# Kernel tuning notes

Measured on AMD Instinct MI355X. Metric: run time of the kernel, lower is better.

## Reference

```python
import jax, jax.numpy as jnp
import numpy as np

N = 100000   # nodes
E = 3200000  # edges
D = 256      # node_dim
H = 64       # hidden (conv1 out)
L = 64       # latent_dim
G = 128      # graphs in batch


def _gcn_conv(x, src, dst, W, b):
    """PyG GCNConv with edge_weight=1: add self-loops, sym deg-norm, scatter-add."""
    n = x.shape[0]
    loop = jnp.arange(n)
    s = jnp.concatenate([src, loop])
    d = jnp.concatenate([dst, loop])
    w = jnp.ones(s.shape[0], x.dtype)
    deg = jax.ops.segment_sum(w, d, num_segments=n)
    dinv = jnp.where(deg > 0, jax.lax.rsqrt(deg), 0.0)
    norm = dinv[s] * w * dinv[d]                      # [E+N]
    h = x @ W                                         # lin (no bias)
    out = jax.ops.segment_sum(h[s] * norm[:, None], d, num_segments=n)
    return out + b


def _mean_pool(z, batch, num_graphs):
    zsum = jax.ops.segment_sum(z, batch, num_segments=num_graphs)
    cnt = jax.ops.segment_sum(jnp.ones(z.shape[0], z.dtype), batch, num_segments=num_graphs)
    return zsum / jnp.clip(cnt, 1.0)[:, None]


def setup_inputs() -> dict:
    key = jax.random.key(0)
    ks = jax.random.split(key, 8)
    x = jax.random.normal(ks[0], (N, D), jnp.float32)
    edge_index = jax.random.randint(ks[1], (2, E), 0, N, dtype=jnp.int64)
    batch = jnp.sort(jax.random.randint(ks[2], (N,), 0, G, dtype=jnp.int64))
    glorot = lambda k, fi, fo: jax.random.normal(k, (fi, fo), jnp.float32) / np.sqrt(fi).astype(np.float32)
    return {
        "x": x, "edge_index": edge_index, "batch": batch,
        "W1": glorot(ks[3], D, H), "b1": jnp.zeros((H,), jnp.float32),
        "W2": glorot(ks[4], H, L), "b2": jnp.zeros((L,), jnp.float32),
        "Wd1": glorot(ks[5], L, 64), "bd1": jnp.zeros((64,), jnp.float32),
        "Wd2": glorot(ks[6], 64, D), "bd2": jnp.zeros((D,), jnp.float32),
    }


def reference(x, edge_index, batch, W1, b1, W2, b2, Wd1, bd1, Wd2, bd2):
    src, dst = edge_index[0], edge_index[1]
    h = jax.nn.relu(_gcn_conv(x, src, dst, W1, b1))
    z = _gcn_conv(h, src, dst, W2, b2)
    z_pool = _mean_pool(z, batch, G)                  # [G, L]
    x_hat = jax.nn.relu(z_pool @ Wd1 + bd1) @ Wd2 + bd2  # [G, D]
    return (x_hat, z_pool)
```

## Files before the change

### kernel.cpp

```cpp
#include <hip/hip_runtime.h>
#include <hip/hip_bf16.h>
#include <hip/hip_fp16.h>
#include <hip/hip_fp8.h>

namespace {
constexpr int kN = 100000;
constexpr int kE = 3200000;
constexpr int kD = 256;
constexpr int kH = 64;
constexpr int kG = 128;

constexpr int kNB   = 782;
constexpr int kCapS = 4608;
constexpr int kCap  = 64;
constexpr int kNPad = 100352;

constexpr size_t kSlBytes = (size_t)(kN + 1) * 32;

constexpr size_t kAlign = 512;
constexpr size_t align_up(size_t v) { return (v + kAlign - 1) & ~(kAlign - 1); }

constexpr size_t OFF_CURD = 0;
constexpr size_t OFF_GCNT = OFF_CURD + align_up(kNB * 4);
constexpr size_t OFF_QRAW = OFF_GCNT + kAlign;
constexpr size_t ZERO_BYTES = OFF_QRAW + align_up((size_t)kG * kH * 4);
constexpr size_t OFF_CNT  = ZERO_BYTES;
constexpr size_t OFF_DINV = OFF_CNT + align_up((size_t)kNPad * 4);
constexpr size_t OFF_SD   = OFF_DINV + align_up((size_t)kNPad * 4);
constexpr size_t OFF_REC  = OFF_SD + align_up((size_t)kNB * kCapS * 4);
constexpr size_t OFF_HL   = OFF_REC + align_up((size_t)kNPad * kCap * 4);
constexpr size_t OFF_H2   = OFF_HL + align_up(2 * kSlBytes);
}

__device__ __forceinline__ unsigned pack4_fp8(float a, float b, float c, float d) {
#if __has_builtin(__builtin_amdgcn_cvt_pk_fp8_f32)
    int r = 0;
    r = __builtin_amdgcn_cvt_pk_fp8_f32(a, b, r, false);
    r = __builtin_amdgcn_cvt_pk_fp8_f32(c, d, r, true);
    return (unsigned)r;
#else
    __hip_fp8_e4m3 qa(a), qb(b), qc(c), qd(d);
    return (unsigned)qa.__x | ((unsigned)qb.__x << 8)
         | ((unsigned)qc.__x << 16) | ((unsigned)qd.__x << 24);
#endif
}

__device__ __forceinline__ void add4q(float (&acc)[4], unsigned u) {
#if __has_builtin(__builtin_amdgcn_cvt_pk_f32_fp8)
    typedef float v2f __attribute__((ext_vector_type(2)));
    v2f f0 = __builtin_amdgcn_cvt_pk_f32_fp8((int)u, false);
    v2f f1 = __builtin_amdgcn_cvt_pk_f32_fp8((int)u, true);
    acc[0] += f0.x; acc[1] += f0.y; acc[2] += f1.x; acc[3] += f1.y;
#else
    #pragma unroll
    for (int j = 0; j < 4; ++j) {
        __hip_fp8_e4m3 v; v.__x = (__hip_fp8_storage_t)((u >> (8 * j)) & 0xFF);
        acc[j] += (float)v;
    }
#endif
}

__global__ __launch_bounds__(1024) void k_bucket(const int* __restrict__ src,
                                                 const int* __restrict__ dst,
                                                 int* __restrict__ curD,
                                                 unsigned* __restrict__ streamD) {
    __shared__ int cD[kNB], bD[kNB];
    int t = threadIdx.x;
    for (int i = t; i < kNB; i += 1024) cD[i] = 0;
    __syncthreads();
    int e0 = blockIdx.x * 16384;
    #pragma unroll
    for (int k = 0; k < 16; ++k) {
        int e = e0 + k * 1024 + t;
        if (e < kE) atomicAdd(&cD[dst[e] >> 7], 1);
    }
    __syncthreads();
    for (int i = t; i < kNB; i += 1024)
        bD[i] = cD[i] ? atomicAdd(&curD[i], cD[i]) : 0;
    __syncthreads();
    for (int i = t; i < kNB; i += 1024) cD[i] = 0;
    __syncthreads();
    #pragma unroll
    for (int k = 0; k < 16; ++k) {
        int e = e0 + k * 1024 + t;
        if (e < kE) {
            int s = src[e], d = dst[e];
            int pd = bD[d >> 7] + atomicAdd(&cD[d >> 7], 1);
            if (pd < kCapS)
                streamD[(size_t)(d >> 7) * kCapS + pd] =
                    ((unsigned)(d & 127) << 17) | (unsigned)s;
        }
    }
}

__global__ __launch_bounds__(256) void k_fillB(const int* __restrict__ curD,
                                               const unsigned* __restrict__ streamD,
                                               int* __restrict__ rec,
                                               int* __restrict__ cnt) {
    __shared__ int lc[128];
    int b = blockIdx.x, t = threadIdx.x;
    if (t < 128) lc[t] = 0;
    __syncthreads();
    int n = min(curD[b], kCapS);
    const unsigned* sp = streamD + (size_t)b * kCapS;
    for (int i = t; i < n; i += 256) {
        unsigned u = sp[i];
        int dlo = (u >> 17) & 127;
        int slot = atomicAdd(&lc[dlo], 1);
        if (slot < kCap)
            rec[((((size_t)b << 7) | dlo) << 6) + slot] = (int)(u & 0x1FFFF);
    }
    __syncthreads();
    if (t < 128) {
        int d = (b << 7) + t;
        if (d < kNPad) cnt[d] = lc[t];
    }
}

__global__ void k_gcnt(const int* __restrict__ batch, int* __restrict__ gcnt) {
    __shared__ int h[kG];
    int t = threadIdx.x;
    if (t < kG) h[t] = 0;
    __syncthreads();
    for (int i = blockIdx.x * blockDim.x + t; i < kN; i += gridDim.x * blockDim.x)
        atomicAdd(&h[batch[i]], 1);
    __syncthreads();
    if (t < kG && h[t]) atomicAdd(&gcnt[t], h[t]);
}

__global__ void k_dinv(const int* __restrict__ cnt, float* __restrict__ dinv,
                       unsigned* __restrict__ hl8, unsigned* __restrict__ h8) {
    int i = blockIdx.x * blockDim.x + threadIdx.x;
    if (i < kN) dinv[i] = rsqrtf((float)(cnt[i] + 1));
    if (blockIdx.x == 0 && threadIdx.x < 32) {
        int t = threadIdx.x;
        unsigned* p = (t < 16) ? hl8 : h8;
        int s = (t >> 3) & 1;
        int j = t & 7;
        p[(s * kSlBytes) / 4 + (size_t)kN * 8 + j] = 0u;
    }
}

__global__ __launch_bounds__(256) void k_gemm1(const float* __restrict__ x,
                                               const float* __restrict__ W1,
                                               const float* __restrict__ dinv,
                                               unsigned char* __restrict__ hl8) {
    constexpr int TM = 64;
    constexpr int KC = 32;
    __shared__ float xs[TM][36];
    __shared__ float ws[KC][kH];
    int t = threadIdx.x;
    int tx = t & 15;
    int ty = t >> 4;
    int nb = blockIdx.x * TM;
    float acc[4][4] = {};
    for (int k0 = 0; k0 < kD; k0 += KC) {
        #pragma unroll
        for (int j = 0; j < 2; ++j) {
            int id = t * 2 + j;
            int row = id >> 3;
            int c4 = (id & 7) * 4;
            int node = nb + row;
            if (node >= kN) node = kN - 1;
            float4 v = *(const float4*)(x + (size_t)node * kD + k0 + c4);
            *(float4*)&xs[row][c4] = v;
        }
        #pragma unroll
        for (int j = 0; j < 2; ++j) {
            int id = t * 2 + j;
            int row = id >> 4;
            int c4 = (id & 15) * 4;
            float4 v = *(const float4*)(W1 + (size_t)(k0 + row) * kH + c4);
            *(float4*)&ws[row][c4] = v;
        }
        __syncthreads();
        #pragma unroll
        for (int kk = 0; kk < KC; ++kk) {
            float a0 = xs[ty * 4 + 0][kk];
            float a1 = xs[ty * 4 + 1][kk];
            float a2 = xs[ty * 4 + 2][kk];
            float a3 = xs[ty * 4 + 3][kk];
            float4 b = *(const float4*)&ws[kk][tx * 4];
            acc[0][0] = fmaf(a0, b.x, acc[0][0]); acc[0][1] = fmaf(a0, b.y, acc[0][1]);
            acc[0][2] = fmaf(a0, b.z, acc[0][2]); acc[0][3] = fmaf(a0, b.w, acc[0][3]);
            acc[1][0] = fmaf(a1, b.x, acc[1][0]); acc[1][1] = fmaf(a1, b.y, acc[1][1]);
            acc[1][2] = fmaf(a1, b.z, acc[1][2]); acc[1][3] = fmaf(a1, b.w, acc[1][3]);
            acc[2][0] = fmaf(a2, b.x, acc[2][0]); acc[2][1] = fmaf(a2, b.y, acc[2][1]);
            acc[2][2] = fmaf(a2, b.z, acc[2][2]); acc[2][3] = fmaf(a2, b.w, acc[2][3]);
            acc[3][0] = fmaf(a3, b.x, acc[3][0]); acc[3][1] = fmaf(a3, b.y, acc[3][1]);
            acc[3][2] = fmaf(a3, b.z, acc[3][2]); acc[3][3] = fmaf(a3, b.w, acc[3][3]);
        }
        __syncthreads();
    }
    int slice = tx >> 3;
    int off = (tx & 7) * 4;
    #pragma unroll
    for (int i = 0; i < 4; ++i) {
        int node = nb + ty * 4 + i;
        if (node < kN) {
            float di = dinv[node];
            unsigned p = pack4_fp8(di * acc[i][0], di * acc[i][1],
                                   di * acc[i][2], di * acc[i][3]);
            *(unsigned*)(hl8 + slice * kSlBytes + (size_t)node * 32 + off) = p;
        }
    }
}

__global__ __launch_bounds__(256) void k_conv1(const int* __restrict__ rec,
                                               const int* __restrict__ cnt,
                                               const float* __restrict__ dinv,
                                               const unsigned char* __restrict__ hl8,
                                               const float* __restrict__ b1,
                                               unsigned char* __restrict__ h8) {
    int tid = threadIdx.x;
    int lane = tid & 63;
    int slice = blockIdx.x & 1;
    int node = (blockIdx.x >> 1) * 4 + (tid >> 6);
    if (node >= kN) return;
    int slot = lane >> 3;
    int fl = lane & 7;
    const unsigned char* hsl = hl8 + slice * kSlBytes;
    size_t base = (size_t)node << 6;
    int len = min(cnt[node], kCap);
    float a0[4] = {}, a1[4] = {};
    for (int c0 = 0; c0 < len; c0 += 16) {
        int e0 = c0 + slot;
        int e1 = c0 + 8 + slot;
        int s0 = (e0 < len) ? rec[base + e0] : kN;
        int s1 = (e1 < len) ? rec[base + e1] : kN;
        unsigned v0 = *(const unsigned*)(hsl + (size_t)s0 * 32 + fl * 4);
        unsigned v1 = *(const unsigned*)(hsl + (size_t)s1 * 32 + fl * 4);
        add4q(a0, v0);
        add4q(a1, v1);
    }
    #pragma unroll
    for (int j = 0; j < 4; ++j) a0[j] += a1[j];
    #pragma unroll
    for (int d = 8; d < 64; d <<= 1) {
        #pragma unroll
        for (int j = 0; j < 4; ++j) a0[j] += __shfl_xor(a0[j], d, 64);
    }
    if (slot == 0) {
        unsigned sv = *(const unsigned*)(hsl + (size_t)node * 32 + fl * 4);
        add4q(a0, sv);
        float di = dinv[node];
        float4 bz = *(const float4*)(b1 + slice * 32 + fl * 4);
        float r0 = di * fmaxf(fmaf(di, a0[0], bz.x), 0.f);
        float r1 = di * fmaxf(fmaf(di, a0[1], bz.y), 0.f);
        float r2 = di * fmaxf(fmaf(di, a0[2], bz.z), 0.f);
        float r3 = di * fmaxf(fmaf(di, a0[3], bz.w), 0.f);
        unsigned o = pack4_fp8(r0, r1, r2, r3);
        *(unsigned*)(h8 + slice * kSlBytes + (size_t)node * 32 + fl * 4) = o;
    }
}

__global__ __launch_bounds__(256) void k_pool3(const int* __restrict__ rec,
                                               const int* __restrict__ cnt,
                                               const float* __restrict__ dinv,
                                               const unsigned char* __restrict__ h8,
                                               const int* __restrict__ batch,
                                               float* __restrict__ q_raw) {
    constexpr int CHUNK = 8;
    int tid = threadIdx.x;
    int lane = tid & 63;
    int slice = blockIdx.x & 1;
    int wid = (blockIdx.x >> 1) * 4 + (tid >> 6);
    int n0 = wid * CHUNK;
    if (n0 >= kN) return;
    int n1 = n0 + CHUNK; if (n1 > kN) n1 = kN;
    int slot = lane >> 3;
    int fl = lane & 7;
    const unsigned char* hsl = h8 + slice * kSlBytes;
    float racc[4] = {};
    int gcur = batch[n0];
    for (int i = n0; i < n1; ++i) {
        int g = batch[i];
        if (g != gcur) {
            #pragma unroll
            for (int d = 8; d < 64; d <<= 1) {
                #pragma unroll
                for (int j = 0; j < 4; ++j) racc[j] += __shfl_xor(racc[j], d, 64);
            }
            if (lane < 8) {
                #pragma unroll
                for (int j = 0; j < 4; ++j)
                    atomicAdd(&q_raw[(gcur << 6) + slice * 32 + fl * 4 + j], racc[j]);
            }
            #pragma unroll
            for (int j = 0; j < 4; ++j) racc[j] = 0.f;
            gcur = g;
        }
        size_t base = (size_t)i << 6;
        int len = min(cnt[i], kCap);
        float ns0[4] = {}, ns1[4] = {};
        for (int c0 = 0; c0 < len; c0 += 16) {
            int e0 = c0 + slot;
            int e1 = c0 + 8 + slot;
            int s0 = (e0 < len) ? rec[base + e0] : kN;
            int s1 = (e1 < len) ? rec[base + e1] : kN;
            unsigned v0 = *(const unsigned*)(hsl + (size_t)s0 * 32 + fl * 4);
            unsigned v1 = *(const unsigned*)(hsl + (size_t)s1 * 32 + fl * 4);
            add4q(ns0, v0);
            add4q(ns1, v1);
        }
        if (slot == 0) {
            unsigned sv = *(const unsigned*)(hsl + (size_t)i * 32 + fl * 4);
            add4q(ns0, sv);
        }
        float di = dinv[i];
        #pragma unroll
        for (int j = 0; j < 4; ++j) racc[j] = fmaf(di, ns0[j] + ns1[j], racc[j]);
    }
    #pragma unroll
    for (int d = 8; d < 64; d <<= 1) {
        #pragma unroll
        for (int j = 0; j < 4; ++j) racc[j] += __shfl_xor(racc[j], d, 64);
    }
    if (lane < 8) {
        #pragma unroll
        for (int j = 0; j < 4; ++j)
            atomicAdd(&q_raw[(gcur << 6) + slice * 32 + fl * 4 + j], racc[j]);
    }
}

__global__ __launch_bounds__(64) void k_head(const float* __restrict__ q_raw,
                                             const int* __restrict__ gcnt,
                                             const float* __restrict__ W2,
                                             const float* __restrict__ b2,
                                             const float* __restrict__ Wd1,
                                             const float* __restrict__ bd1,
                                             const float* __restrict__ Wd2,
                                             const float* __restrict__ bd2,
                                             float* __restrict__ out) {
    __shared__ float zm[kH], zp[kH], tt[kH];
    int g = blockIdx.x, c = threadIdx.x;
    int cg = gcnt[g];
    float inv = (cg > 0) ? 1.f / (float)cg : 0.f;
    zm[c] = q_raw[(size_t)g * kH + c] * inv;
    __syncthreads();
    float a = b2[c];
    #pragma unroll 8
    for (int k = 0; k < kH; ++k) a = fmaf(zm[k], W2[k * kH + c], a);
    if (cg == 0) a = 0.f;
    out[(size_t)kG * kD + (size_t)g * kH + c] = a;
    zp[c] = a;
    __syncthreads();
    float t = bd1[c];
    #pragma unroll 8
    for (int k = 0; k < kH; ++k) t = fmaf(zp[k], Wd1[k * 64 + c], t);
    tt[c] = fmaxf(t, 0.f);
    __syncthreads();
    #pragma unroll
    for (int j4 = 0; j4 < 4; ++j4) {
        int col = c + j4 * 64;
        float v = bd2[col];
        #pragma unroll 8
        for (int k = 0; k < 64; ++k) v = fmaf(tt[k], Wd2[k * kD + col], v);
        out[(size_t)g * kD + col] = v;
    }
}

extern "C" void kernel_launch(void* const* d_in, const int* in_sizes, int n_in,
                              void* d_out, int out_size, void* d_ws, size_t ws_size,
                              hipStream_t stream) {
    const float* x    = (const float*)d_in[0];
    const int*   ei   = (const int*)d_in[1];
    const int*   src  = ei;
    const int*   dst  = ei + kE;
    const int*   batch= (const int*)d_in[2];
    const float* W1   = (const float*)d_in[3];
    const float* b1   = (const float*)d_in[4];
    const float* W2   = (const float*)d_in[5];
    const float* b2   = (const float*)d_in[6];
    const float* Wd1  = (const float*)d_in[7];
    const float* bd1  = (const float*)d_in[8];
    const float* Wd2  = (const float*)d_in[9];
    const float* bd2  = (const float*)d_in[10];
    float* out = (float*)d_out;

    char* ws = (char*)d_ws;
    int*           curD  = (int*)(ws + OFF_CURD);
    int*           gcnt  = (int*)(ws + OFF_GCNT);
    float*         q_raw = (float*)(ws + OFF_QRAW);
    int*           cnt   = (int*)(ws + OFF_CNT);
    float*         dinv  = (float*)(ws + OFF_DINV);
    unsigned*      sD    = (unsigned*)(ws + OFF_SD);
    int*           rec   = (int*)(ws + OFF_REC);
    unsigned char* hl8   = (unsigned char*)(ws + OFF_HL);
    unsigned char* h8    = (unsigned char*)(ws + OFF_H2);

    hipMemsetAsync(d_ws, 0, ZERO_BYTES, stream);

    const int nBucketBlocks = (kE + 16383) / 16384;

    k_bucket<<<nBucketBlocks, 1024, 0, stream>>>(src, dst, curD, sD);
    k_fillB<<<kNB, 256, 0, stream>>>(curD, sD, rec, cnt);

    k_gcnt<<<128, 256, 0, stream>>>(batch, gcnt);
    k_dinv<<<(kN + 255) / 256, 256, 0, stream>>>(cnt, dinv,
                                                 (unsigned*)hl8, (unsigned*)h8);

    k_gemm1<<<(kN + 63) / 64, 256, 0, stream>>>(x, W1, dinv, hl8);

    k_conv1<<<((kN + 3) / 4) * 2, 256, 0, stream>>>(rec, cnt, dinv, hl8, b1, h8);

    const int nPoolWaves = (kN + 7) / 8;
    k_pool3<<<((nPoolWaves + 3) / 4) * 2, 256, 0, stream>>>(rec, cnt, dinv, h8, batch, q_raw);

    k_head<<<kG, 64, 0, stream>>>(q_raw, gcnt, W2, b2, Wd1, bd1, Wd2, bd2, out);
}
```

Measured before the change: 319.1 us.

## Store conv1 input as unsliced 64-byte fp8 rows and gather full rows

```diff
diff --git a/kernel.cpp b/kernel.cpp
--- a/kernel.cpp
+++ b/kernel.cpp
@@ -29,7 +29,7 @@
 constexpr size_t OFF_SD   = OFF_DINV + align_up((size_t)kNPad * 4);
 constexpr size_t OFF_REC  = OFF_SD + align_up((size_t)kNB * kCapS * 4);
 constexpr size_t OFF_HL   = OFF_REC + align_up((size_t)kNPad * kCap * 4);
-constexpr size_t OFF_H2   = OFF_HL + align_up(2 * kSlBytes);
+constexpr size_t OFF_H2   = OFF_HL + align_up((size_t)(kN + 1) * kH);
 }
 
 __device__ __forceinline__ unsigned pack4_fp8(float a, float b, float c, float d) {
@@ -60,6 +60,13 @@
 #endif
 }
 
+__device__ __forceinline__ void add8q(float (&acc)[8], uint2 u) {
+    float* a0 = acc;
+    float* a1 = acc + 4;
+    add4q(*(float(*)[4])a0, u.x);
+    add4q(*(float(*)[4])a1, u.y);
+}
+
 __global__ __launch_bounds__(1024) void k_bucket(const int* __restrict__ src,
                                                  const int* __restrict__ dst,
                                                  int* __restrict__ curD,
@@ -134,10 +141,13 @@
     if (i < kN) dinv[i] = rsqrtf((float)(cnt[i] + 1));
     if (blockIdx.x == 0 && threadIdx.x < 32) {
         int t = threadIdx.x;
-        unsigned* p = (t < 16) ? hl8 : h8;
-        int s = (t >> 3) & 1;
-        int j = t & 7;
-        p[(s * kSlBytes) / 4 + (size_t)kN * 8 + j] = 0u;
+        if (t < 16) {
+            hl8[(size_t)kN * 16 + t] = 0u;
+        } else {
+            int s = (t >> 3) & 1;
+            int j = t & 7;
+            h8[(s * kSlBytes) / 4 + (size_t)kN * 8 + j] = 0u;
+        }
     }
 }
 
@@ -147,7 +157,7 @@
                                                unsigned char* __restrict__ hl8) {
     constexpr int TM = 64;
     constexpr int KC = 32;
-    __shared__ float xs[TM][36];
+    __shared__ float xs[KC][TM + 4];
     __shared__ float ws[KC][kH];
     int t = threadIdx.x;
     int tx = t & 15;
@@ -163,7 +173,10 @@
             int node = nb + row;
             if (node >= kN) node = kN - 1;
             float4 v = *(const float4*)(x + (size_t)node * kD + k0 + c4);
-            *(float4*)&xs[row][c4] = v;
+            xs[c4 + 0][row] = v.x;
+            xs[c4 + 1][row] = v.y;
+            xs[c4 + 2][row] = v.z;
+            xs[c4 + 3][row] = v.w;
         }
         #pragma unroll
         for (int j = 0; j < 2; ++j) {
@@ -176,24 +189,19 @@
         __syncthreads();
         #pragma unroll
         for (int kk = 0; kk < KC; ++kk) {
-            float a0 = xs[ty * 4 + 0][kk];
-            float a1 = xs[ty * 4 + 1][kk];
-            float a2 = xs[ty * 4 + 2][kk];
-            float a3 = xs[ty * 4 + 3][kk];
+            float4 a = *(const float4*)&xs[kk][ty * 4];
             float4 b = *(const float4*)&ws[kk][tx * 4];
-            acc[0][0] = fmaf(a0, b.x, acc[0][0]); acc[0][1] = fmaf(a0, b.y, acc[0][1]);
-            acc[0][2] = fmaf(a0, b.z, acc[0][2]); acc[0][3] = fmaf(a0, b.w, acc[0][3]);
-            acc[1][0] = fmaf(a1, b.x, acc[1][0]); acc[1][1] = fmaf(a1, b.y, acc[1][1]);
-            acc[1][2] = fmaf(a1, b.z, acc[1][2]); acc[1][3] = fmaf(a1, b.w, acc[1][3]);
-            acc[2][0] = fmaf(a2, b.x, acc[2][0]); acc[2][1] = fmaf(a2, b.y, acc[2][1]);
-            acc[2][2] = fmaf(a2, b.z, acc[2][2]); acc[2][3] = fmaf(a2, b.w, acc[2][3]);
-            acc[3][0] = fmaf(a3, b.x, acc[3][0]); acc[3][1] = fmaf(a3, b.y, acc[3][1]);
-            acc[3][2] = fmaf(a3, b.z, acc[3][2]); acc[3][3] = fmaf(a3, b.w, acc[3][3]);
+            acc[0][0] = fmaf(a.x, b.x, acc[0][0]); acc[0][1] = fmaf(a.x, b.y, acc[0][1]);
+            acc[0][2] = fmaf(a.x, b.z, acc[0][2]); acc[0][3] = fmaf(a.x, b.w, acc[0][3]);
+            acc[1][0] = fmaf(a.y, b.x, acc[1][0]); acc[1][1] = fmaf(a.y, b.y, acc[1][1]);
+            acc[1][2] = fmaf(a.y, b.z, acc[1][2]); acc[1][3] = fmaf(a.y, b.w, acc[1][3]);
+            acc[2][0] = fmaf(a.z, b.x, acc[2][0]); acc[2][1] = fmaf(a.z, b.y, acc[2][1]);
+            acc[2][2] = fmaf(a.z, b.z, acc[2][2]); acc[2][3] = fmaf(a.z, b.w, acc[2][3]);
+            acc[3][0] = fmaf(a.w, b.x, acc[3][0]); acc[3][1] = fmaf(a.w, b.y, acc[3][1]);
+            acc[3][2] = fmaf(a.w, b.z, acc[3][2]); acc[3][3] = fmaf(a.w, b.w, acc[3][3]);
         }
         __syncthreads();
     }
-    int slice = tx >> 3;
-    int off = (tx & 7) * 4;
     #pragma unroll
     for (int i = 0; i < 4; ++i) {
         int node = nb + ty * 4 + i;
@@ -201,7 +209,7 @@
             float di = dinv[node];
             unsigned p = pack4_fp8(di * acc[i][0], di * acc[i][1],
                                    di * acc[i][2], di * acc[i][3]);
-            *(unsigned*)(hl8 + slice * kSlBytes + (size_t)node * 32 + off) = p;
+            *(unsigned*)(hl8 + (size_t)node * kH + tx * 4) = p;
         }
     }
 }
@@ -214,43 +222,45 @@
                                                unsigned char* __restrict__ h8) {
     int tid = threadIdx.x;
     int lane = tid & 63;
-    int slice = blockIdx.x & 1;
-    int node = (blockIdx.x >> 1) * 4 + (tid >> 6);
+    int node = blockIdx.x * 4 + (tid >> 6);
     if (node >= kN) return;
     int slot = lane >> 3;
     int fl = lane & 7;
-    const unsigned char* hsl = hl8 + slice * kSlBytes;
     size_t base = (size_t)node << 6;
     int len = min(cnt[node], kCap);
-    float a0[4] = {}, a1[4] = {};
+    float acc0[8] = {}, acc1[8] = {};
     for (int c0 = 0; c0 < len; c0 += 16) {
         int e0 = c0 + slot;
         int e1 = c0 + 8 + slot;
         int s0 = (e0 < len) ? rec[base + e0] : kN;
         int s1 = (e1 < len) ? rec[base + e1] : kN;
-        unsigned v0 = *(const unsigned*)(hsl + (size_t)s0 * 32 + fl * 4);
-        unsigned v1 = *(const unsigned*)(hsl + (size_t)s1 * 32 + fl * 4);
-        add4q(a0, v0);
-        add4q(a1, v1);
-    }
-    #pragma unroll
-    for (int j = 0; j < 4; ++j) a0[j] += a1[j];
+        uint2 v0 = *(const uint2*)(hl8 + ((size_t)s0 << 6) + fl * 8);
+        uint2 v1 = *(const uint2*)(hl8 + ((size_t)s1 << 6) + fl * 8);
+        add8q(acc0, v0);
+        add8q(acc1, v1);
+    }
+    #pragma unroll
+    for (int j = 0; j < 8; ++j) acc0[j] += acc1[j];
     #pragma unroll
     for (int d = 8; d < 64; d <<= 1) {
         #pragma unroll
-        for (int j = 0; j < 4; ++j) a0[j] += __shfl_xor(a0[j], d, 64);
+        for (int j = 0; j < 8; ++j) acc0[j] += __shfl_xor(acc0[j], d, 64);
     }
     if (slot == 0) {
-        unsigned sv = *(const unsigned*)(hsl + (size_t)node * 32 + fl * 4);
-        add4q(a0, sv);
+        uint2 sv = *(const uint2*)(hl8 + ((size_t)node << 6) + fl * 8);
+        add8q(acc0, sv);
         float di = dinv[node];
-        float4 bz = *(const float4*)(b1 + slice * 32 + fl * 4);
-        float r0 = di * fmaxf(fmaf(di, a0[0], bz.x), 0.f);
-        float r1 = di * fmaxf(fmaf(di, a0[1], bz.y), 0.f);
-        float r2 = di * fmaxf(fmaf(di, a0[2], bz.z), 0.f);
-        float r3 = di * fmaxf(fmaf(di, a0[3], bz.w), 0.f);
-        unsigned o = pack4_fp8(r0, r1, r2, r3);
-        *(unsigned*)(h8 + slice * kSlBytes + (size_t)node * 32 + fl * 4) = o;
+        float4 ba = *(const float4*)(b1 + fl * 8);
+        float4 bb = *(const float4*)(b1 + fl * 8 + 4);
+        float bz[8] = {ba.x, ba.y, ba.z, ba.w, bb.x, bb.y, bb.z, bb.w};
+        float r[8];
+        #pragma unroll
+        for (int j = 0; j < 8; ++j)
+            r[j] = di * fmaxf(fmaf(di, acc0[j], bz[j]), 0.f);
+        uint2 o;
+        o.x = pack4_fp8(r[0], r[1], r[2], r[3]);
+        o.y = pack4_fp8(r[4], r[5], r[6], r[7]);
+        *(uint2*)(h8 + (size_t)(fl >> 2) * kSlBytes + (size_t)node * 32 + (fl & 3) * 8) = o;
     }
 }
 
@@ -402,7 +412,7 @@
 
     k_gemm1<<<(kN + 63) / 64, 256, 0, stream>>>(x, W1, dinv, hl8);
 
-    k_conv1<<<((kN + 3) / 4) * 2, 256, 0, stream>>>(rec, cnt, dinv, hl8, b1, h8);
+    k_conv1<<<(kN + 3) / 4, 256, 0, stream>>>(rec, cnt, dinv, hl8, b1, h8);
 
     const int nPoolWaves = (kN + 7) / 8;
     k_pool3<<<((nPoolWaves + 3) / 4) * 2, 256, 0, stream>>>(rec, cnt, dinv, h8, batch, q_raw);
```

Result: faster. 293.6 us (median of 2 runs) (-8.0%).
